# Kernel optimization log

Measured on AMD Instinct MI355X. Metric: run time of the kernel, lower is better.

Reference implementation:

```python
import jax, jax.numpy as jnp
import numpy as np
import math

V, T, D, N, H, DFF = 32000, 1024, 1024, 6, 16, 4096
DK = D // H
EPS = 1e-6


def setup_inputs() -> dict:
    key = jax.random.key(0)
    ks = jax.random.split(key, 20)
    s = 0.02
    B = 2
    return {
        "idx": jax.random.randint(ks[0], (B, T), 0, V, dtype=jnp.int32),
        "emb": jax.random.normal(ks[1], (V, D), jnp.float32) * s,
        # attention projections, stored [in, out] so y = x @ W
        "Wq": jax.random.normal(ks[2], (N, D, D), jnp.float32) * s,
        "Wk": jax.random.normal(ks[3], (N, D, D), jnp.float32) * s,
        "Wv": jax.random.normal(ks[4], (N, D, D), jnp.float32) * s,
        "Wo": jax.random.normal(ks[5], (N, D, D), jnp.float32) * s,
        "ln1_a": jnp.ones((N, D), jnp.float32),
        "ln1_b": jnp.zeros((N, D), jnp.float32),
        "ln2_a": jnp.ones((N, D), jnp.float32),
        "ln2_b": jnp.zeros((N, D), jnp.float32),
        "W1": jax.random.normal(ks[6], (N, D, DFF), jnp.float32) * s,
        "b1": jnp.zeros((N, DFF), jnp.float32),
        "W2": jax.random.normal(ks[7], (N, DFF, D), jnp.float32) * s,
        "b2": jnp.zeros((N, D), jnp.float32),
        "fnorm_a": jnp.ones((D,), jnp.float32),
        "fnorm_b": jnp.zeros((D,), jnp.float32),
        "Wp": jax.random.normal(ks[8], (D, V), jnp.float32) * s,
        "bp": jnp.zeros((V,), jnp.float32),
    }


def _layernorm(x, a, b):
    # torch .std() uses Bessel correction (ddof=1); denom is (std + eps), not sqrt(var+eps)
    mean = x.mean(axis=-1, keepdims=True)
    std = jnp.std(x, axis=-1, keepdims=True, ddof=1)
    return a * (x - mean) / (std + EPS) + b


def _pos_encoding(t, d):
    pos = jnp.arange(t, dtype=jnp.float32)[:, None]
    div = jnp.exp(jnp.arange(0, d, 2, dtype=jnp.float32) * (-math.log(10000.0) / d))
    pe = jnp.zeros((t, d), jnp.float32)
    pe = pe.at[:, 0::2].set(jnp.sin(pos * div))
    pe = pe.at[:, 1::2].set(jnp.cos(pos * div))
    return pe


def _forward(idx, emb, Wq, Wk, Wv, Wo, ln1_a, ln1_b, ln2_a, ln2_b,
             W1, b1, W2, b2, fnorm_a, fnorm_b, Wp, bp):
    B, Tc = idx.shape
    x = emb[idx] * math.sqrt(D) + _pos_encoding(Tc, D)  # [B,T,D]
    causal = jnp.tril(jnp.ones((Tc, Tc), bool))  # [T,T]

    def block(x, p):
        wq, wk, wv, wo, a1, c1, a2, c2, w1, bb1, w2, bb2 = p
        h_in = _layernorm(x, a1, c1)
        q = (h_in @ wq).reshape(B, Tc, H, DK).transpose(0, 2, 1, 3)
        k = (h_in @ wk).reshape(B, Tc, H, DK).transpose(0, 2, 1, 3)
        v = (h_in @ wv).reshape(B, Tc, H, DK).transpose(0, 2, 1, 3)
        scores = jnp.einsum('bhqd,bhkd->bhqk', q, k) / math.sqrt(DK)
        scores = jnp.where(causal, scores, -1e9)
        attn = jax.nn.softmax(scores, axis=-1)
        o = jnp.einsum('bhqk,bhkd->bhqd', attn, v)
        o = o.transpose(0, 2, 1, 3).reshape(B, Tc, D) @ wo
        x = x + o
        h2 = _layernorm(x, a2, c2)
        ff = jax.nn.relu(h2 @ w1 + bb1) @ w2 + bb2
        x = x + ff
        return x, None

    x, _ = jax.lax.scan(block, x, (Wq, Wk, Wv, Wo, ln1_a, ln1_b, ln2_a, ln2_b, W1, b1, W2, b2))
    x = _layernorm(x, fnorm_a, fnorm_b)
    logits = x @ Wp + bp  # [B,T,V]
    return logits


def reference(idx, emb, Wq, Wk, Wv, Wo, ln1_a, ln1_b, ln2_a, ln2_b,
              W1, b1, W2, b2, fnorm_a, fnorm_b, Wp, bp):
    return _forward(idx, emb, Wq, Wk, Wv, Wo, ln1_a, ln1_b, ln2_a, ln2_b,
                    W1, b1, W2, b2, fnorm_a, fnorm_b, Wp, bp)
```

## Files before the change

kernel.cpp:

```cpp
#include <hip/hip_runtime.h>
#include <hip/hip_bf16.h>
#include <math.h>

#define VOCAB 32000
#define TSEQ 1024
#define DMODEL 1024
#define NLAYERS 6
#define NHEADS 16
#define DFF 4096
#define DKH 64
#define BATCH 2
#define MROWS (BATCH * TSEQ)
#define LN_EPS 1e-6f
#define QKVS 3072

typedef unsigned short u16;
typedef __attribute__((ext_vector_type(8))) short short8v;
typedef __attribute__((ext_vector_type(4))) float f32x4;

__device__ __forceinline__ u16 f2bb(float f) {
    __hip_bfloat16 h = __float2bfloat16(f);
    u16 u; __builtin_memcpy(&u, &h, 2); return u;
}

__device__ __forceinline__ void gload16(const void* g, void* l) {
    __builtin_amdgcn_global_load_lds(
        (const __attribute__((address_space(1))) unsigned int*)g,
        (__attribute__((address_space(3))) unsigned int*)l, 16, 0, 0);
}

__global__ void embed_kernel(const int* __restrict__ idx,
                             const float* __restrict__ emb,
                             float* __restrict__ x) {
    int i = blockIdx.x * blockDim.x + threadIdx.x;
    if (i >= MROWS * DMODEL) return;
    int row = i / DMODEL;
    int d = i - row * DMODEL;
    int t = row % TSEQ;
    int tok = idx[row];
    float e = emb[(size_t)tok * DMODEL + d] * 32.0f;
    float freq = expf(-(float)(d & ~1) * (9.210340371976184f / (float)DMODEL));
    float ang = (float)t * freq;
    float pe = (d & 1) ? cosf(ang) : sinf(ang);
    x[i] = e + pe;
}

template<bool OB16>
__global__ void __launch_bounds__(256) ln_kernel(const float* __restrict__ x,
                                                 const float* __restrict__ a,
                                                 const float* __restrict__ b,
                                                 void* __restrict__ yv) {
    __shared__ float red[8];
    int row = blockIdx.x;
    int tid = threadIdx.x;
    float4 v = ((const float4*)(x + (size_t)row * DMODEL))[tid];
    float s = v.x + v.y + v.z + v.w;
    #pragma unroll
    for (int off = 32; off; off >>= 1) s += __shfl_xor(s, off, 64);
    if ((tid & 63) == 0) red[tid >> 6] = s;
    __syncthreads();
    float mean = (red[0] + red[1] + red[2] + red[3]) * (1.0f / DMODEL);
    float dx = v.x - mean, dy = v.y - mean, dz = v.z - mean, dw = v.w - mean;
    float ss = dx * dx + dy * dy + dz * dz + dw * dw;
    #pragma unroll
    for (int off = 32; off; off >>= 1) ss += __shfl_xor(ss, off, 64);
    if ((tid & 63) == 0) red[4 + (tid >> 6)] = ss;
    __syncthreads();
    float var = (red[4] + red[5] + red[6] + red[7]) * (1.0f / (DMODEL - 1));
    float inv = 1.0f / (sqrtf(var) + LN_EPS);
    const float4 a4 = ((const float4*)a)[tid];
    const float4 b4 = ((const float4*)b)[tid];
    float o0 = a4.x * dx * inv + b4.x;
    float o1 = a4.y * dy * inv + b4.y;
    float o2 = a4.z * dz * inv + b4.z;
    float o3 = a4.w * dw * inv + b4.w;
    if (OB16) {
        ushort4 o; o.x = f2bb(o0); o.y = f2bb(o1); o.z = f2bb(o2); o.w = f2bb(o3);
        ((ushort4*)((u16*)yv + (size_t)row * DMODEL))[tid] = o;
    } else {
        float4 o; o.x = o0; o.y = o1; o.z = o2; o.w = o3;
        ((float4*)((float*)yv + (size_t)row * DMODEL))[tid] = o;
    }
}

__global__ void __launch_bounds__(256) convT(const float* __restrict__ in,
                                             u16* __restrict__ out, int K, int N) {
    __shared__ float t[32][33];
    in  += (size_t)blockIdx.z * K * N;
    out += (size_t)blockIdx.z * K * N;
    const int tx = threadIdx.x, ty = threadIdx.y;
    const int n0 = blockIdx.x * 32, k0 = blockIdx.y * 32;
    #pragma unroll
    for (int i = 0; i < 4; ++i)
        t[ty + i * 8][tx] = in[(size_t)(k0 + ty + i * 8) * N + n0 + tx];
    __syncthreads();
    #pragma unroll
    for (int i = 0; i < 4; ++i)
        out[(size_t)(n0 + ty + i * 8) * K + k0 + tx] = f2bb(t[tx][ty + i * 8]);
}

__global__ void __launch_bounds__(256) convQKVO(const float* __restrict__ Wq,
                                                const float* __restrict__ Wk,
                                                const float* __restrict__ Wv,
                                                const float* __restrict__ Wo,
                                                u16* __restrict__ WqkvT,
                                                u16* __restrict__ WoT) {
    __shared__ float t[32][33];
    const int z = blockIdx.z, L = z >> 2, p = z & 3;
    const size_t MM = (size_t)DMODEL * DMODEL;
    const float* in = (p == 0 ? Wq : p == 1 ? Wk : p == 2 ? Wv : Wo) + (size_t)L * MM;
    u16* out = (p < 3) ? (WqkvT + (size_t)L * 3 * MM + (size_t)p * MM)
                       : (WoT + (size_t)L * MM);
    const int tx = threadIdx.x, ty = threadIdx.y;
    const int n0 = blockIdx.x * 32, k0 = blockIdx.y * 32;
    #pragma unroll
    for (int i = 0; i < 4; ++i)
        t[ty + i * 8][tx] = in[(size_t)(k0 + ty + i * 8) * DMODEL + n0 + tx];
    __syncthreads();
    #pragma unroll
    for (int i = 0; i < 4; ++i)
        out[(size_t)(n0 + ty + i * 8) * DMODEL + k0 + tx] = f2bb(t[tx][ty + i * 8]);
}

template<int BMT, bool BIAS, bool RELU, bool RES, bool OB16, bool NT>
__global__ void __launch_bounds__(256) gemm_mfma(
    const u16* __restrict__ A, const u16* __restrict__ Bt,
    const float* __restrict__ bias, const float* res,
    void* outp, int N, int K)
{
    constexpr int MR = BMT / 32;
    constexpr int AR = BMT / 64;
    __shared__ u16 Alds[BMT * 32];
    __shared__ u16 Blds[128 * 32];
    const int tid = threadIdx.x;
    const int w = tid >> 6, lane = tid & 63;
    const int wr = w >> 1, wc = w & 1;
    const size_t bm = (size_t)blockIdx.y * BMT;
    const size_t bn = (size_t)blockIdx.x * 128;
    const int srow = (w << 4) + (lane >> 2);
    const int scol = (((lane & 3) ^ ((lane >> 3) & 3)) << 3);
    const int fr = lane & 15, fq = lane >> 4;
    const int aswz = ((fq ^ ((fr >> 1) & 3)) << 3);

    f32x4 acc[MR][4];
    #pragma unroll
    for (int m = 0; m < MR; ++m)
        #pragma unroll
        for (int n = 0; n < 4; ++n)
            acc[m][n] = (f32x4){0.f, 0.f, 0.f, 0.f};

    for (int k0 = 0; k0 < K; k0 += 32) {
        #pragma unroll
        for (int li = 0; li < AR; ++li)
            gload16(A + (bm + li * 64 + srow) * K + k0 + scol, Alds + li * 2048 + w * 512);
        #pragma unroll
        for (int li = 0; li < 2; ++li)
            gload16(Bt + (bn + li * 64 + srow) * K + k0 + scol, Blds + li * 2048 + w * 512);
        __syncthreads();
        short8v a[MR], b[4];
        #pragma unroll
        for (int m = 0; m < MR; ++m)
            a[m] = *(const short8v*)(Alds + (wr * (BMT / 2) + m * 16 + fr) * 32 + aswz);
        #pragma unroll
        for (int n = 0; n < 4; ++n)
            b[n] = *(const short8v*)(Blds + (wc * 64 + n * 16 + fr) * 32 + aswz);
        #pragma unroll
        for (int m = 0; m < MR; ++m)
            #pragma unroll
            for (int n = 0; n < 4; ++n)
                acc[m][n] = __builtin_amdgcn_mfma_f32_16x16x32_bf16(a[m], b[n], acc[m][n], 0, 0, 0);
        __syncthreads();
    }

    #pragma unroll
    for (int n = 0; n < 4; ++n) {
        const size_t col = bn + wc * 64 + n * 16 + fr;
        const float bv = BIAS ? bias[col] : 0.f;
        #pragma unroll
        for (int m = 0; m < MR; ++m) {
            #pragma unroll
            for (int r = 0; r < 4; ++r) {
                const size_t row = bm + wr * (BMT / 2) + m * 16 + fq * 4 + r;
                float v = acc[m][n][r] + bv;
                if (RELU) v = fmaxf(v, 0.f);
                if (RES)  v += res[row * N + col];
                if (OB16) ((u16*)outp)[row * N + col] = f2bb(v);
                else if (NT) __builtin_nontemporal_store(v, (float*)outp + row * N + col);
                else      ((float*)outp)[row * N + col] = v;
            }
        }
    }
}

__global__ void __launch_bounds__(256) attn_flash(const u16* __restrict__ qkv,
                                                  u16* __restrict__ o) {
    __shared__ u16 Klds[64 * 64];
    __shared__ u16 Vt[64 * 64];
    __shared__ u16 Plds[4][16 * 72];

    const int tid = threadIdx.x;
    const int w = tid >> 6, lane = tid & 63;
    const int fr = lane & 15, fq = lane >> 4;
    const int qt = blockIdx.x, h = blockIdx.y, b = blockIdx.z;
    const int qbase = qt * 64 + w * 16;
    const size_t rowbase = (size_t)b * TSEQ;
    const int hd = h * DKH;

    const u16* qrow = qkv + (rowbase + qbase + fr) * QKVS + hd;
    const short8v qf0 = *(const short8v*)(qrow + fq * 8);
    const short8v qf1 = *(const short8v*)(qrow + 32 + fq * 8);

    float m[4], l[4];
    f32x4 oa[4];
    #pragma unroll
    for (int r = 0; r < 4; ++r) { m[r] = -1e30f; l[r] = 0.f; }
    #pragma unroll
    for (int nd = 0; nd < 4; ++nd) oa[nd] = (f32x4){0.f, 0.f, 0.f, 0.f};

    for (int t = 0; t <= qt; ++t) {
        const int j0 = t * 64;
        #pragma unroll
        for (int half = 0; half < 2; ++half) {
            const int r = (tid >> 3) + half * 32;
            const int c8 = (tid & 7) << 3;
            const size_t grow = (rowbase + j0 + r) * QKVS + hd + c8;
            short8v kv = *(const short8v*)(qkv + grow + 1024);
            int kbyte = (r * 128 + c8 * 2) ^ ((r & 7) << 4);
            *(short8v*)((char*)Klds + kbyte) = kv;
            short8v vv = *(const short8v*)(qkv + grow + 2048);
            #pragma unroll
            for (int i = 0; i < 8; ++i) {
                const int vrow = c8 + i;
                const int slot = ((r >> 3) + (vrow >> 3)) & 7;
                Vt[vrow * 64 + slot * 8 + (r & 7)] = (u16)vv[i];
            }
        }
        __syncthreads();

        f32x4 s[4];
        __builtin_amdgcn_s_setprio(1);
        #pragma unroll
        for (int ct = 0; ct < 4; ++ct) {
            const int krow = ct * 16 + fr;
            const int swz = (krow & 7) << 4;
            short8v k0 = *(const short8v*)((char*)Klds + ((krow * 128 + fq * 16) ^ swz));
            short8v k1 = *(const short8v*)((char*)Klds + ((krow * 128 + 64 + fq * 16) ^ swz));
            f32x4 a = (f32x4){0.f, 0.f, 0.f, 0.f};
            a = __builtin_amdgcn_mfma_f32_16x16x32_bf16(qf0, k0, a, 0, 0, 0);
            a = __builtin_amdgcn_mfma_f32_16x16x32_bf16(qf1, k1, a, 0, 0, 0);
            s[ct] = a;
        }
        __builtin_amdgcn_s_setprio(0);

        float c[4];
        #pragma unroll
        for (int r = 0; r < 4; ++r) {
            const int qg = qbase + fq * 4 + r;
            float sv[4];
            #pragma unroll
            for (int ct = 0; ct < 4; ++ct) {
                sv[ct] = s[ct][r] * 0.125f;
                if (j0 + ct * 16 + fr > qg) sv[ct] = -1e30f;
            }
            float mx = fmaxf(fmaxf(sv[0], sv[1]), fmaxf(sv[2], sv[3]));
            mx = fmaxf(mx, __shfl_xor(mx, 1, 64));
            mx = fmaxf(mx, __shfl_xor(mx, 2, 64));
            mx = fmaxf(mx, __shfl_xor(mx, 4, 64));
            mx = fmaxf(mx, __shfl_xor(mx, 8, 64));
            const float mn = fmaxf(m[r], mx);
            c[r] = __expf(m[r] - mn);
            m[r] = mn;
            float p0 = __expf(sv[0] - mn);
            float p1 = __expf(sv[1] - mn);
            float p2 = __expf(sv[2] - mn);
            float p3 = __expf(sv[3] - mn);
            float rs = (p0 + p1) + (p2 + p3);
            rs += __shfl_xor(rs, 1, 64);
            rs += __shfl_xor(rs, 2, 64);
            rs += __shfl_xor(rs, 4, 64);
            rs += __shfl_xor(rs, 8, 64);
            l[r] = l[r] * c[r] + rs;
            u16* prow = &Plds[w][(fq * 4 + r) * 72];
            prow[fr]      = f2bb(p0);
            prow[16 + fr] = f2bb(p1);
            prow[32 + fr] = f2bb(p2);
            prow[48 + fr] = f2bb(p3);
        }
        #pragma unroll
        for (int nd = 0; nd < 4; ++nd)
            #pragma unroll
            for (int r = 0; r < 4; ++r)
                oa[nd][r] *= c[r];
        asm volatile("s_waitcnt lgkmcnt(0)" ::: "memory");
        __builtin_amdgcn_sched_barrier(0);

        __builtin_amdgcn_s_setprio(1);
        #pragma unroll
        for (int ks = 0; ks < 2; ++ks) {
            const short8v pf = *(const short8v*)(&Plds[w][fr * 72 + ks * 32 + fq * 8]);
            #pragma unroll
            for (int nd = 0; nd < 4; ++nd) {
                const int vrow = nd * 16 + fr;
                const int slot = (ks * 4 + fq + (vrow >> 3)) & 7;
                const short8v vf = *(const short8v*)(&Vt[vrow * 64 + slot * 8]);
                oa[nd] = __builtin_amdgcn_mfma_f32_16x16x32_bf16(pf, vf, oa[nd], 0, 0, 0);
            }
        }
        __builtin_amdgcn_s_setprio(0);
        __syncthreads();
    }

    #pragma unroll
    for (int r = 0; r < 4; ++r) {
        const float inv = 1.0f / l[r];
        u16* orow = o + (rowbase + qbase + fq * 4 + r) * DMODEL + hd;
        #pragma unroll
        for (int nd = 0; nd < 4; ++nd)
            orow[nd * 16 + fr] = f2bb(oa[nd][r] * inv);
    }
}

#define FBM 64
#define FBN 64
#define FBK 16
__global__ void __launch_bounds__(256) gemm_f32(
    const float* __restrict__ A, const float* __restrict__ Bw,
    const float* __restrict__ bias, float* outp, int N, int K)
{
    __shared__ float As[FBK][FBM];
    __shared__ float Bs[FBK][FBN];
    const int bm = blockIdx.y * FBM, bn = blockIdx.x * FBN;
    const int tid = threadIdx.x;
    const int tr = (tid >> 4) << 2, tc = (tid & 15) << 2;
    const int am = tid >> 2, ak = (tid & 3) << 2;
    const int bk = tid >> 4, bn4 = (tid & 15) << 2;
    float acc[4][4] = {};
    const float* Ap = A + (size_t)(bm + am) * K + ak;
    const float* Bp = Bw + (size_t)bk * N + bn + bn4;
    for (int k0 = 0; k0 < K; k0 += FBK) {
        float4 av = *(const float4*)(Ap + k0);
        float4 bv = *(const float4*)(Bp + (size_t)k0 * N);
        As[ak + 0][am] = av.x; As[ak + 1][am] = av.y; As[ak + 2][am] = av.z; As[ak + 3][am] = av.w;
        *(float4*)&Bs[bk][bn4] = bv;
        __syncthreads();
        #pragma unroll
        for (int kk = 0; kk < FBK; ++kk) {
            float4 a4 = *(const float4*)&As[kk][tr];
            float4 b4 = *(const float4*)&Bs[kk][tc];
            acc[0][0] += a4.x*b4.x; acc[0][1] += a4.x*b4.y; acc[0][2] += a4.x*b4.z; acc[0][3] += a4.x*b4.w;
            acc[1][0] += a4.y*b4.x; acc[1][1] += a4.y*b4.y; acc[1][2] += a4.y*b4.z; acc[1][3] += a4.y*b4.w;
            acc[2][0] += a4.z*b4.x; acc[2][1] += a4.z*b4.y; acc[2][2] += a4.z*b4.z; acc[2][3] += a4.z*b4.w;
            acc[3][0] += a4.w*b4.x; acc[3][1] += a4.w*b4.y; acc[3][2] += a4.w*b4.z; acc[3][3] += a4.w*b4.w;
        }
        __syncthreads();
    }
    #pragma unroll
    for (int i = 0; i < 4; ++i) {
        int row = bm + tr + i;
        float4 o;
        o.x = acc[i][0] + bias[bn + tc + 0];
        o.y = acc[i][1] + bias[bn + tc + 1];
        o.z = acc[i][2] + bias[bn + tc + 2];
        o.w = acc[i][3] + bias[bn + tc + 3];
        *(float4*)(outp + (size_t)row * N + bn + tc) = o;
    }
}

extern "C" void kernel_launch(void* const* d_in, const int* in_sizes, int n_in,
                              void* d_out, int out_size, void* d_ws, size_t ws_size,
                              hipStream_t stream) {
    const int* idx = (const int*)d_in[0];
    const float* emb = (const float*)d_in[1];
    const float* Wq = (const float*)d_in[2];
    const float* Wk = (const float*)d_in[3];
    const float* Wv = (const float*)d_in[4];
    const float* Wo = (const float*)d_in[5];
    const float* ln1a = (const float*)d_in[6];
    const float* ln1b = (const float*)d_in[7];
    const float* ln2a = (const float*)d_in[8];
    const float* ln2b = (const float*)d_in[9];
    const float* W1 = (const float*)d_in[10];
    const float* b1 = (const float*)d_in[11];
    const float* W2 = (const float*)d_in[12];
    const float* b2 = (const float*)d_in[13];
    const float* fa = (const float*)d_in[14];
    const float* fb = (const float*)d_in[15];
    const float* Wp = (const float*)d_in[16];
    const float* bp = (const float*)d_in[17];
    float* out = (float*)d_out;

    const size_t MD = (size_t)MROWS * DMODEL;
    const size_t MM = (size_t)DMODEL * DMODEL;
    u16* U = (u16*)out;
    u16* qkv = U;
    u16* ob = U + 3 * MD;
    u16* hb = U + 4 * MD;
    float* x = (float*)(U + 5 * MD);
    u16* ff = U + 7 * MD;
    u16* WqkvT = U + 12 * MD;
    u16* WoT = U + 21 * MD;
    u16* W1T = U + 24 * MD;
    u16* W2T = U + 36 * MD;

    const bool pathA = ws_size >= (size_t)68 * 1024 * 1024 + 256;
    u16* WpT = (u16*)d_ws;
    u16* h2b = (u16*)((char*)d_ws + (size_t)64 * 1024 * 1024);
    float* hF = (float*)d_ws;

    dim3 cblk(32, 8);
    convQKVO<<<dim3(32, 32, 24), cblk, 0, stream>>>(Wq, Wk, Wv, Wo, WqkvT, WoT);
    convT<<<dim3(128, 32, 6), cblk, 0, stream>>>(W1, W1T, DMODEL, DFF);
    convT<<<dim3(32, 128, 6), cblk, 0, stream>>>(W2, W2T, DFF, DMODEL);
    if (pathA) convT<<<dim3(1000, 32, 1), cblk, 0, stream>>>(Wp, WpT, DMODEL, VOCAB);

    embed_kernel<<<(MROWS * DMODEL + 255) / 256, 256, 0, stream>>>(idx, emb, x);

    for (int L = 0; L < NLAYERS; ++L) {
        ln_kernel<true><<<MROWS, 256, 0, stream>>>(x, ln1a + (size_t)L * DMODEL, ln1b + (size_t)L * DMODEL, hb);
        gemm_mfma<128, false, false, false, true, false><<<dim3(24, 16), 256, 0, stream>>>(
            hb, WqkvT + (size_t)L * 3 * MM, nullptr, nullptr, qkv, QKVS, DMODEL);
        attn_flash<<<dim3(TSEQ / 64, NHEADS, BATCH), 256, 0, stream>>>(qkv, ob);
        gemm_mfma<64, false, false, true, false, false><<<dim3(8, 32), 256, 0, stream>>>(
            ob, WoT + (size_t)L * MM, nullptr, x, x, DMODEL, DMODEL);
        ln_kernel<true><<<MROWS, 256, 0, stream>>>(x, ln2a + (size_t)L * DMODEL, ln2b + (size_t)L * DMODEL, hb);
        gemm_mfma<128, true, true, false, true, false><<<dim3(32, 16), 256, 0, stream>>>(
            hb, W1T + (size_t)L * DFF * DMODEL, b1 + (size_t)L * DFF, nullptr, ff, DFF, DMODEL);
        gemm_mfma<64, true, false, true, false, false><<<dim3(8, 32), 256, 0, stream>>>(
            ff, W2T + (size_t)L * DFF * DMODEL, b2 + (size_t)L * DMODEL, x, x, DMODEL, DFF);
    }

    if (pathA) {
        ln_kernel<true><<<MROWS, 256, 0, stream>>>(x, fa, fb, h2b);
        gemm_mfma<128, true, false, false, false, true><<<dim3(250, 16), 256, 0, stream>>>(
            h2b, WpT, bp, nullptr, out, VOCAB, DMODEL);
    } else {
        ln_kernel<false><<<MROWS, 256, 0, stream>>>(x, fa, fb, hF);
        gemm_f32<<<dim3(VOCAB / FBN, MROWS / FBM), 256, 0, stream>>>(hF, Wp, bp, out, VOCAB, DMODEL);
    }
}
```

Measured before the change: 1.768 ms.

## Fuse per-layer LayerNorm into GEMM A-tile loading, drop nontemporal logits store

The two per-layer LayerNorm kernels are removed. The QKV and W1 GEMMs now read the fp32 residual stream directly: each block first computes per-row mean and inverse std, then normalizes, converts to bf16 and writes into the swizzled LDS A tile on every k-step. This saves the launches and the bf16 round trip through global memory. In exchange, every N-tile block (24 or 32 per row band) recomputes the row statistics and reads fp32 activations, twice the bytes of bf16, with synchronous loads in place of async gload. The final vocab projection also switches from nontemporal to ordinary stores.

```diff
diff --git a/kernel.cpp b/kernel.cpp
--- a/kernel.cpp
+++ b/kernel.cpp
@@ -122,16 +122,21 @@
         out[(size_t)(n0 + ty + i * 8) * DMODEL + k0 + tx] = f2bb(t[tx][ty + i * 8]);
 }
 
-template<int BMT, bool BIAS, bool RELU, bool RES, bool OB16, bool NT>
+template<int BMT, bool BIAS, bool RELU, bool RES, bool OB16, bool LNA>
 __global__ void __launch_bounds__(256) gemm_mfma(
-    const u16* __restrict__ A, const u16* __restrict__ Bt,
+    const void* __restrict__ Ap_, const u16* __restrict__ Bt,
     const float* __restrict__ bias, const float* res,
-    void* outp, int N, int K)
+    void* outp, const float* __restrict__ lna, const float* __restrict__ lnb,
+    int N, int K)
 {
     constexpr int MR = BMT / 32;
     constexpr int AR = BMT / 64;
     __shared__ u16 Alds[BMT * 32];
     __shared__ u16 Blds[128 * 32];
+    __shared__ float lnmean[128];
+    __shared__ float lninv[128];
+    const u16* A16 = (const u16*)Ap_;
+    const float* Af = (const float*)Ap_;
     const int tid = threadIdx.x;
     const int w = tid >> 6, lane = tid & 63;
     const int wr = w >> 1, wc = w & 1;
@@ -142,6 +147,30 @@
     const int fr = lane & 15, fq = lane >> 4;
     const int aswz = ((fq ^ ((fr >> 1) & 3)) << 3);
 
+    if constexpr (LNA) {
+        const int r = tid >> 1, half = tid & 1;
+        const float* xr = Af + (bm + r) * (size_t)K + half * (K / 2);
+        float s = 0.f;
+        for (int i = 0; i < K / 2; i += 4) {
+            float4 v = *(const float4*)(xr + i);
+            s += (v.x + v.y) + (v.z + v.w);
+        }
+        s += __shfl_xor(s, 1, 64);
+        const float mean = s / (float)K;
+        float ss = 0.f;
+        for (int i = 0; i < K / 2; i += 4) {
+            float4 v = *(const float4*)(xr + i);
+            float d0 = v.x - mean, d1 = v.y - mean, d2 = v.z - mean, d3 = v.w - mean;
+            ss += (d0 * d0 + d1 * d1) + (d2 * d2 + d3 * d3);
+        }
+        ss += __shfl_xor(ss, 1, 64);
+        if (!half) {
+            lnmean[r] = mean;
+            lninv[r] = 1.0f / (sqrtf(ss * (1.0f / (K - 1))) + LN_EPS);
+        }
+        __syncthreads();
+    }
+
     f32x4 acc[MR][4];
     #pragma unroll
     for (int m = 0; m < MR; ++m)
@@ -150,9 +179,37 @@
             acc[m][n] = (f32x4){0.f, 0.f, 0.f, 0.f};
 
     for (int k0 = 0; k0 < K; k0 += 32) {
-        #pragma unroll
-        for (int li = 0; li < AR; ++li)
-            gload16(A + (bm + li * 64 + srow) * K + k0 + scol, Alds + li * 2048 + w * 512);
+        if constexpr (LNA) {
+            const int r = tid >> 1;
+            const int jb = (tid & 1) * 2;
+            const float mean = lnmean[r], inv = lninv[r];
+            const float* xr = Af + (bm + r) * (size_t)K + k0 + jb * 8;
+            #pragma unroll
+            for (int j = 0; j < 2; ++j) {
+                const int c0 = k0 + (jb + j) * 8;
+                float4 v0 = *(const float4*)(xr + j * 8);
+                float4 v1 = *(const float4*)(xr + j * 8 + 4);
+                float4 a0 = *(const float4*)(lna + c0);
+                float4 a1 = *(const float4*)(lna + c0 + 4);
+                float4 g0 = *(const float4*)(lnb + c0);
+                float4 g1 = *(const float4*)(lnb + c0 + 4);
+                short8v pk;
+                pk[0] = (short)f2bb((v0.x - mean) * inv * a0.x + g0.x);
+                pk[1] = (short)f2bb((v0.y - mean) * inv * a0.y + g0.y);
+                pk[2] = (short)f2bb((v0.z - mean) * inv * a0.z + g0.z);
+                pk[3] = (short)f2bb((v0.w - mean) * inv * a0.w + g0.w);
+                pk[4] = (short)f2bb((v1.x - mean) * inv * a1.x + g1.x);
+                pk[5] = (short)f2bb((v1.y - mean) * inv * a1.y + g1.y);
+                pk[6] = (short)f2bb((v1.z - mean) * inv * a1.z + g1.z);
+                pk[7] = (short)f2bb((v1.w - mean) * inv * a1.w + g1.w);
+                const int pb = (jb + j) ^ (((r & 15) >> 1) & 3);
+                *(short8v*)(Alds + r * 32 + pb * 8) = pk;
+            }
+        } else {
+            #pragma unroll
+            for (int li = 0; li < AR; ++li)
+                gload16(A16 + (bm + li * 64 + srow) * K + k0 + scol, Alds + li * 2048 + w * 512);
+        }
         #pragma unroll
         for (int li = 0; li < 2; ++li)
             gload16(Bt + (bn + li * 64 + srow) * K + k0 + scol, Blds + li * 2048 + w * 512);
@@ -185,7 +242,6 @@
                 if (RELU) v = fmaxf(v, 0.f);
                 if (RES)  v += res[row * N + col];
                 if (OB16) ((u16*)outp)[row * N + col] = f2bb(v);
-                else if (NT) __builtin_nontemporal_store(v, (float*)outp + row * N + col);
                 else      ((float*)outp)[row * N + col] = v;
             }
         }
@@ -394,7 +450,6 @@
     u16* U = (u16*)out;
     u16* qkv = U;
     u16* ob = U + 3 * MD;
-    u16* hb = U + 4 * MD;
     float* x = (float*)(U + 5 * MD);
     u16* ff = U + 7 * MD;
     u16* WqkvT = U + 12 * MD;
@@ -416,23 +471,24 @@
     embed_kernel<<<(MROWS * DMODEL + 255) / 256, 256, 0, stream>>>(idx, emb, x);
 
     for (int L = 0; L < NLAYERS; ++L) {
-        ln_kernel<true><<<MROWS, 256, 0, stream>>>(x, ln1a + (size_t)L * DMODEL, ln1b + (size_t)L * DMODEL, hb);
-        gemm_mfma<128, false, false, false, true, false><<<dim3(24, 16), 256, 0, stream>>>(
-            hb, WqkvT + (size_t)L * 3 * MM, nullptr, nullptr, qkv, QKVS, DMODEL);
+        gemm_mfma<128, false, false, false, true, true><<<dim3(24, 16), 256, 0, stream>>>(
+            x, WqkvT + (size_t)L * 3 * MM, nullptr, nullptr, qkv,
+            ln1a + (size_t)L * DMODEL, ln1b + (size_t)L * DMODEL, QKVS, DMODEL);
         attn_flash<<<dim3(TSEQ / 64, NHEADS, BATCH), 256, 0, stream>>>(qkv, ob);
         gemm_mfma<64, false, false, true, false, false><<<dim3(8, 32), 256, 0, stream>>>(
-            ob, WoT + (size_t)L * MM, nullptr, x, x, DMODEL, DMODEL);
-        ln_kernel<true><<<MROWS, 256, 0, stream>>>(x, ln2a + (size_t)L * DMODEL, ln2b + (size_t)L * DMODEL, hb);
-        gemm_mfma<128, true, true, false, true, false><<<dim3(32, 16), 256, 0, stream>>>(
-            hb, W1T + (size_t)L * DFF * DMODEL, b1 + (size_t)L * DFF, nullptr, ff, DFF, DMODEL);
+            ob, WoT + (size_t)L * MM, nullptr, x, x, nullptr, nullptr, DMODEL, DMODEL);
+        gemm_mfma<128, true, true, false, true, true><<<dim3(32, 16), 256, 0, stream>>>(
+            x, W1T + (size_t)L * DFF * DMODEL, b1 + (size_t)L * DFF, nullptr, ff,
+            ln2a + (size_t)L * DMODEL, ln2b + (size_t)L * DMODEL, DFF, DMODEL);
         gemm_mfma<64, true, false, true, false, false><<<dim3(8, 32), 256, 0, stream>>>(
-            ff, W2T + (size_t)L * DFF * DMODEL, b2 + (size_t)L * DMODEL, x, x, DMODEL, DFF);
+            ff, W2T + (size_t)L * DFF * DMODEL, b2 + (size_t)L * DMODEL, x, x,
+            nullptr, nullptr, DMODEL, DFF);
     }
 
     if (pathA) {
         ln_kernel<true><<<MROWS, 256, 0, stream>>>(x, fa, fb, h2b);
-        gemm_mfma<128, true, false, false, false, true><<<dim3(250, 16), 256, 0, stream>>>(
-            h2b, WpT, bp, nullptr, out, VOCAB, DMODEL);
+        gemm_mfma<128, true, false, false, false, false><<<dim3(250, 16), 256, 0, stream>>>(
+            h2b, WpT, bp, nullptr, out, nullptr, nullptr, VOCAB, DMODEL);
     } else {
         ln_kernel<false><<<MROWS, 256, 0, stream>>>(x, fa, fb, hF);
         gemm_f32<<<dim3(VOCAB / FBN, MROWS / FBM), 256, 0, stream>>>(hF, Wp, bp, out, VOCAB, DMODEL);
```

After: 3.182 ms. 1.8x slower.
